# Optimization experiments

Measured on AMD Instinct MI355X. Metric: run time of the kernel, lower is better.

The kernel has to match this reference:

```python
import jax, jax.numpy as jnp
import numpy as np

C, K, D_LLM = 32, 16, 768
B, L, D_MODEL = 8, 512, 256
H, D_KEYS = 8, 32
TEMP = 1.0 / np.sqrt(D_KEYS)


def setup_inputs() -> dict:
    key = jax.random.key(0)
    ks = jax.random.split(key, 8)
    topk = jax.random.normal(ks[0], (C, K, D_LLM), dtype=jnp.float32)
    ts_emb = jax.random.normal(ks[1], (B, L, D_MODEL), dtype=jnp.float32)
    probs = jax.random.uniform(ks[2], (B, L, C), dtype=jnp.float32)
    probs = probs / jnp.sum(probs, axis=-1, keepdims=True)  # soft cluster probabilities
    scale = 0.02  # keep pre-softmax logits in a stable range
    q_proj = jax.random.normal(ks[3], (C, H * D_KEYS, D_MODEL + 1), dtype=jnp.float32) * scale
    k_proj = jax.random.normal(ks[4], (C, H * D_KEYS, D_LLM + 1), dtype=jnp.float32) * scale
    v_proj = jax.random.normal(ks[5], (C, H * D_KEYS, D_LLM + 1), dtype=jnp.float32) * scale
    out_w = jax.random.normal(ks[6], (C, H, D_KEYS, D_LLM), dtype=jnp.float32) * scale
    out_b = jax.random.normal(ks[7], (C, D_LLM), dtype=jnp.float32) * scale
    return {"topk_token_embeddings": topk, "ts_emb": ts_emb, "cluster_probs": probs,
            "q_proj": q_proj, "k_proj": k_proj, "v_proj": v_proj,
            "out_w": out_w, "out_b": out_b}


def reference(topk_token_embeddings, ts_emb, cluster_probs, q_proj, k_proj, v_proj, out_w, out_b):
    b, l, _ = ts_emb.shape
    c, k, d_llm = topk_token_embeddings.shape
    # per-cluster Q/K/V projections (weights have an extra trailing bias column)
    q = jnp.einsum('bld,cgd->blcg', ts_emb, q_proj[..., :-1]) + q_proj[..., -1]
    q = q.reshape(b, l, c, H, D_KEYS)
    kk = jnp.einsum('ckd,cgd->kcg', topk_token_embeddings, k_proj[..., :-1]) + k_proj[..., -1]
    kk = kk.reshape(k, c, H, D_KEYS)
    v = jnp.einsum('ckd,cgd->kcg', topk_token_embeddings, v_proj[..., :-1]) + v_proj[..., -1]
    v = v.reshape(k, c, H, D_KEYS)
    # cross attention over the k retrieved tokens, per cluster and head
    att = jnp.einsum('blchd,kchd->bchlk', q, kk)  # (B,c,H,L,k)
    att = jax.nn.softmax(TEMP * att, axis=-1)  # dropout disabled (eval)
    out_v = jnp.einsum('bchlk,kchd->bclhd', att, v)
    aligned = jnp.einsum('bclhd,chde->blce', out_v, out_w) + out_b  # (B,L,c,d_llm)
    fused = jnp.sum(aligned * cluster_probs[:, :, :, None], axis=-2)  # (B,L,d_llm)
    return fused
```

## Files before the change

kernel.cpp:

```cpp
#include <hip/hip_runtime.h>
#include <hip/hip_bf16.h>

#define C_   32
#define K_   16
#define DLLM 768
#define DM   256
#define H_   8
#define DK   32
#define G_   256
#define BL   4096
#define NN   4096
#define E_   768
#define LDP  4160
#define TEMPF 0.17677669529663687f
#define SCL2  0.2550348647f

typedef __attribute__((ext_vector_type(8))) short bf16x8;
typedef __attribute__((ext_vector_type(4))) float f32x4;
typedef unsigned int u32;

__device__ __forceinline__ unsigned short f2bf(float f) {
    unsigned int u = __float_as_uint(f);
    unsigned int r = (u + 0x7fffu + ((u >> 16) & 1u)) >> 16;
    return (unsigned short)r;
}
__device__ __forceinline__ float bf2f(unsigned int u) {
    return __uint_as_float(u << 16);
}

__device__ __forceinline__ void gl16(const void* g, void* l) {
    __builtin_amdgcn_global_load_lds(
        (const __attribute__((address_space(1))) u32*)g,
        (__attribute__((address_space(3))) u32*)l, 16, 0, 0);
}

__global__ __launch_bounds__(256) void k1_kv(const float* __restrict__ topk,
                                             const float* __restrict__ kp,
                                             const float* __restrict__ vp,
                                             float* __restrict__ kk,
                                             float* __restrict__ vv) {
    const int c  = blockIdx.x;
    const int gq = blockIdx.y;
    const int t = threadIdx.x;
    const int lane = t & 63, w = t >> 6;

    __shared__ float t_l[K_][DLLM];
    {
        const float4* src = reinterpret_cast<const float4*>(topk + (size_t)c * K_ * DLLM);
        float4* dst = reinterpret_cast<float4*>(&t_l[0][0]);
#pragma unroll
        for (int i = 0; i < 12; ++i)
            dst[t + i * 256] = src[t + i * 256];
    }
    __syncthreads();

    const int g0 = gq * 16 + w * 4;
    const int dbase = lane * 4;

    float4 ck[3], cv[3], nk[3], nv[3];
    {
        const float* kpr = kp + (size_t)(c * G_ + g0) * (DLLM + 1);
        const float* vpr = vp + (size_t)(c * G_ + g0) * (DLLM + 1);
#pragma unroll
        for (int r = 0; r < 3; ++r) {
            ck[r] = *reinterpret_cast<const float4*>(kpr + r * 256 + dbase);
            cv[r] = *reinterpret_cast<const float4*>(vpr + r * 256 + dbase);
        }
    }

#pragma unroll
    for (int gi = 0; gi < 4; ++gi) {
        const int g = g0 + gi;
        const float* kpr = kp + (size_t)(c * G_ + g) * (DLLM + 1);
        const float* vpr = vp + (size_t)(c * G_ + g) * (DLLM + 1);
        if (gi < 3) {
            const float* kpn = kpr + (DLLM + 1);
            const float* vpn = vpr + (DLLM + 1);
#pragma unroll
            for (int r = 0; r < 3; ++r) {
                nk[r] = *reinterpret_cast<const float4*>(kpn + r * 256 + dbase);
                nv[r] = *reinterpret_cast<const float4*>(vpn + r * 256 + dbase);
            }
        }
        const float bk = kpr[DLLM], bv = vpr[DLLM];
        float acck[K_] = {}, accv[K_] = {};
#pragma unroll
        for (int r = 0; r < 3; ++r) {
            const int d = r * 256 + dbase;
#pragma unroll
            for (int k = 0; k < K_; ++k) {
                float4 t4 = *reinterpret_cast<const float4*>(&t_l[k][d]);
                acck[k] += ck[r].x * t4.x + ck[r].y * t4.y + ck[r].z * t4.z + ck[r].w * t4.w;
                accv[k] += cv[r].x * t4.x + cv[r].y * t4.y + cv[r].z * t4.z + cv[r].w * t4.w;
            }
        }
#pragma unroll
        for (int s = 32; s >= 1; s >>= 1) {
#pragma unroll
            for (int k = 0; k < K_; ++k) {
                acck[k] += __shfl_xor(acck[k], s);
                accv[k] += __shfl_xor(accv[k], s);
            }
        }
        if (lane == 0) {
#pragma unroll
            for (int k = 0; k < K_; ++k) {
                kk[(size_t)(c * K_ + k) * G_ + g] = acck[k] + bk;
                vv[(size_t)(c * K_ + k) * G_ + g] = accv[k] + bv;
            }
        }
#pragma unroll
        for (int r = 0; r < 3; ++r) { ck[r] = nk[r]; cv[r] = nv[r]; }
    }
}

__global__ __launch_bounds__(256) void k0_cvt(const float* __restrict__ ts,
                                              const float* __restrict__ probs,
                                              const float* __restrict__ outb,
                                              unsigned short* __restrict__ tsb,
                                              unsigned short* __restrict__ P,
                                              unsigned short* __restrict__ VWt) {
    const int bid = blockIdx.x, t = threadIdx.x;
    if (bid < 1024) {
        const int idx = bid * 1024 + t * 4;
        float4 v = *reinterpret_cast<const float4*>(ts + idx);
        uint2 o;
        o.x = f2bf(v.x) | ((unsigned)f2bf(v.y) << 16);
        o.y = f2bf(v.z) | ((unsigned)f2bf(v.w) << 16);
        *reinterpret_cast<uint2*>(tsb + idx) = o;
    } else if (bid < 1056) {
        const int b2 = bid - 1024;
        const int row = b2 * 128 + (t >> 1);
        const int ch = (t & 1) * 16;
        unsigned short o[16];
#pragma unroll
        for (int j = 0; j < 16; ++j) o[j] = f2bf(probs[row * 32 + ch + j]);
        uint4 u0, u1;
        u0.x = o[0] | (o[1] << 16);  u0.y = o[2] | (o[3] << 16);
        u0.z = o[4] | (o[5] << 16);  u0.w = o[6] | (o[7] << 16);
        u1.x = o[8] | (o[9] << 16);  u1.y = o[10] | (o[11] << 16);
        u1.z = o[12] | (o[13] << 16); u1.w = o[14] | (o[15] << 16);
        unsigned short* dst = P + (size_t)row * LDP + 4096 + ch;
        *reinterpret_cast<uint4*>(dst) = u0;
        *reinterpret_cast<uint4*>(dst + 8) = u1;
        uint4 z = {0u, 0u, 0u, 0u};
        unsigned short* pz = P + (size_t)row * LDP + 4128 + ch;
        *reinterpret_cast<uint4*>(pz) = z;
        *reinterpret_cast<uint4*>(pz + 8) = z;
    } else {
        const int idx = (bid - 1056) * 256 + t;
        const int e = idx >> 5, cc = idx & 31;
        VWt[(size_t)e * LDP + 4096 + cc] = f2bf(outb[cc * E_ + e]);
        VWt[(size_t)e * LDP + 4128 + cc] = 0;
    }
}

__global__ __launch_bounds__(768) void k23(const float* __restrict__ qp,
                                           const float* __restrict__ kk,
                                           const float* __restrict__ ow,
                                           const float* __restrict__ vv,
                                           unsigned short* __restrict__ A2t,
                                           float* __restrict__ abias,
                                           unsigned short* __restrict__ VWt) {
    const int c = blockIdx.x, h = blockIdx.y;
    const int t = threadIdx.x;
    __shared__ float kk_l[K_][DK];
    __shared__ float v_l[K_][DK];
    __shared__ float bq_l[DK];
    if (t < 512) {
        int k = t / DK, d = t % DK;
        kk_l[k][d] = kk[(size_t)(c * K_ + k) * G_ + h * DK + d];
        v_l[k][d]  = vv[(size_t)(c * K_ + k) * G_ + h * DK + d];
    }
    if (t < DK)
        bq_l[t] = qp[(size_t)(c * G_ + h * DK + t) * (DM + 1) + DM];
    __syncthreads();
    const int ch = c * H_ + h;
    {
        const int e = t;
        float acc[K_];
#pragma unroll
        for (int k = 0; k < K_; ++k) acc[k] = 0.f;
        for (int d = 0; d < DK; ++d) {
            float w = ow[((size_t)ch * DK + d) * E_ + e];
#pragma unroll
            for (int k = 0; k < K_; ++k) acc[k] += w * v_l[k][d];
        }
#pragma unroll
        for (int k = 0; k < K_; ++k)
            VWt[(size_t)e * LDP + ch * 16 + k] = f2bf(acc[k]);
    }
    if (t < 256) {
        const int m = t;
        float acc[K_];
#pragma unroll
        for (int k = 0; k < K_; ++k) acc[k] = 0.f;
        for (int d = 0; d < DK; ++d) {
            float wq = qp[(size_t)(c * G_ + h * DK + d) * (DM + 1) + m];
#pragma unroll
            for (int k = 0; k < K_; ++k) acc[k] += wq * kk_l[k][d];
        }
#pragma unroll
        for (int k = 0; k < K_; ++k)
            A2t[(size_t)(ch * 16 + k) * DM + m] = f2bf(acc[k] * SCL2);
        if (m < K_) {
            float s = 0.f;
#pragma unroll
            for (int d = 0; d < DK; ++d) s += bq_l[d] * kk_l[m][d];
            abias[ch * 16 + m] = s * SCL2;
        }
    }
}

__global__ __launch_bounds__(256, 2) void k4_att(const unsigned short* __restrict__ A2t,
                                                 const unsigned short* __restrict__ tsb,
                                                 const float* __restrict__ abias,
                                                 const float* __restrict__ probs,
                                                 unsigned short* __restrict__ P) {
    const int n0  = blockIdx.x * 128;
    const int bl0 = blockIdx.y * 256;
    const int t = threadIdx.x;
    const int lane = t & 63, w = t >> 6;
    const int wr = w >> 1, wc = w & 1;
    const int c = lane & 15, g = lane >> 4;
    const int rsl = (c >> 1) & 3;

    __shared__ unsigned short a_l[3][128 * 32];
    __shared__ unsigned short b_l[3][256 * 32];
    __shared__ float ab_l[128];
    __shared__ float pb_l[256];

    if (t < 128) ab_l[t] = abias[n0 + t];
    pb_l[t] = probs[(size_t)(bl0 + t) * C_ + (n0 >> 7)];

    const int srow = t >> 2;
    const int sw = ((t & 3) ^ ((t >> 3) & 3)) * 8;

#define K4_STAGE(buf, kt)                                                         \
    {                                                                             \
        const int col_ = (kt) * 32 + sw;                                          \
        _Pragma("unroll")                                                         \
        for (int j = 0; j < 2; ++j)                                               \
            gl16(A2t + (size_t)(n0 + j * 64 + srow) * DM + col_,                  \
                 &a_l[buf][j * 2048 + t * 8]);                                    \
        _Pragma("unroll")                                                         \
        for (int j = 0; j < 4; ++j)                                               \
            gl16(tsb + (size_t)(bl0 + j * 64 + srow) * DM + col_,                 \
                 &b_l[buf][j * 2048 + t * 8]);                                    \
    }

    K4_STAGE(0, 0)
    K4_STAGE(1, 1)
    asm volatile("s_waitcnt lgkmcnt(0)" ::: "memory");

    f32x4 acc[4][8] = {};

#pragma unroll
    for (int kt = 0; kt < 8; ++kt) {
        const int bcur = kt % 3;
        if (kt < 6) {
            K4_STAGE((kt + 2) % 3, kt + 2)
            asm volatile("s_waitcnt vmcnt(12)" ::: "memory");
        } else if (kt == 6) {
            asm volatile("s_waitcnt vmcnt(6)" ::: "memory");
        } else {
            asm volatile("s_waitcnt vmcnt(0)" ::: "memory");
        }
        asm volatile("s_barrier" ::: "memory");
        bf16x8 af[4], bfr[8];
#pragma unroll
        for (int a = 0; a < 4; ++a)
            af[a] = *reinterpret_cast<const bf16x8*>(
                &a_l[bcur][(wr * 64 + a * 16 + c) * 32 + (g ^ rsl) * 8]);
#pragma unroll
        for (int b = 0; b < 8; ++b)
            bfr[b] = *reinterpret_cast<const bf16x8*>(
                &b_l[bcur][(wc * 128 + b * 16 + c) * 32 + (g ^ rsl) * 8]);
#pragma unroll
        for (int a = 0; a < 4; ++a)
#pragma unroll
            for (int b = 0; b < 8; ++b)
                acc[a][b] = __builtin_amdgcn_mfma_f32_16x16x32_bf16(af[a], bfr[b], acc[a][b], 0, 0, 0);
        if (kt < 7)
            asm volatile("s_barrier" ::: "memory");
    }
#undef K4_STAGE

#pragma unroll
    for (int a = 0; a < 4; ++a) {
        const int nbase = wr * 64 + a * 16 + g * 4;
#pragma unroll
        for (int b = 0; b < 8; ++b) {
            const int bll = wc * 128 + b * 16 + c;
            float e0 = __builtin_amdgcn_exp2f(acc[a][b][0] + ab_l[nbase + 0]);
            float e1 = __builtin_amdgcn_exp2f(acc[a][b][1] + ab_l[nbase + 1]);
            float e2 = __builtin_amdgcn_exp2f(acc[a][b][2] + ab_l[nbase + 2]);
            float e3 = __builtin_amdgcn_exp2f(acc[a][b][3] + ab_l[nbase + 3]);
            float s = (e0 + e1) + (e2 + e3);
            s += __shfl_xor(s, 16);
            s += __shfl_xor(s, 32);
            const float pv = pb_l[bll] * __builtin_amdgcn_rcpf(s);
            unsigned r0, r1;
            float p0 = e0 * pv, p1 = e1 * pv, p2 = e2 * pv, p3 = e3 * pv;
            asm("v_cvt_pk_bf16_f32 %0, %1, %2" : "=v"(r0) : "v"(p0), "v"(p1));
            asm("v_cvt_pk_bf16_f32 %0, %1, %2" : "=v"(r1) : "v"(p2), "v"(p3));
            uint2 o; o.x = r0; o.y = r1;
            *reinterpret_cast<uint2*>(P + (size_t)(bl0 + bll) * LDP + n0 + nbase) = o;
        }
    }
}

__global__ __launch_bounds__(256, 3) void k5_out(const unsigned short* __restrict__ P,
                                                 const unsigned short* __restrict__ VWt,
                                                 unsigned short* __restrict__ part) {
    const int wg = blockIdx.x;
    const int xcd = wg & 7;
    const int local = wg >> 3;
    const int bl0 = (xcd * 4 + (local & 3)) * 128;
    const int e0  = ((local >> 2) & 3) * 192;
    const int ks  = local >> 4;

    const int t = threadIdx.x;
    const int lane = t & 63, w = t >> 6;
    const int wr = w >> 1, wc = w & 1;
    const int c = lane & 15, g = lane >> 4;
    const int rsl = (c >> 1) & 3;

    __shared__ unsigned short a_l[2][128 * 32];
    __shared__ unsigned short b_l[2][192 * 32];

    const int nstart = ks * 704;
    const int nsteps = (ks == 5) ? 20 : 22;

    const int srow = t >> 2;
    const int sw = ((t & 3) ^ ((t >> 3) & 3)) * 8;

#define K5_STAGE(buf, kt)                                                         \
    {                                                                             \
        const int col_ = nstart + (kt) * 32 + sw;                                 \
        _Pragma("unroll")                                                         \
        for (int j = 0; j < 2; ++j)                                               \
            gl16(P + (size_t)(bl0 + j * 64 + srow) * LDP + col_,                  \
                 &a_l[buf][j * 2048 + t * 8]);                                    \
        _Pragma("unroll")                                                         \
        for (int j = 0; j < 3; ++j)                                               \
            gl16(VWt + (size_t)(e0 + j * 64 + srow) * LDP + col_,                 \
                 &b_l[buf][j * 2048 + t * 8]);                                    \
    }

    K5_STAGE(0, 0)

    f32x4 acc[4][6] = {};
    for (int kt = 0; kt < nsteps; ++kt) {
        const int bcur = kt & 1;
        if (kt + 1 < nsteps) {
            K5_STAGE(bcur ^ 1, kt + 1)
            asm volatile("s_waitcnt vmcnt(5)" ::: "memory");
        } else {
            asm volatile("s_waitcnt vmcnt(0)" ::: "memory");
        }
        asm volatile("s_barrier" ::: "memory");
        bf16x8 af[4], bfr[6];
#pragma unroll
        for (int a = 0; a < 4; ++a)
            af[a] = *reinterpret_cast<const bf16x8*>(
                &a_l[bcur][(wr * 64 + a * 16 + c) * 32 + (g ^ rsl) * 8]);
#pragma unroll
        for (int b = 0; b < 6; ++b)
            bfr[b] = *reinterpret_cast<const bf16x8*>(
                &b_l[bcur][(wc * 96 + b * 16 + c) * 32 + (g ^ rsl) * 8]);
#pragma unroll
        for (int a = 0; a < 4; ++a)
#pragma unroll
            for (int b = 0; b < 6; ++b)
                acc[a][b] = __builtin_amdgcn_mfma_f32_16x16x32_bf16(af[a], bfr[b], acc[a][b], 0, 0, 0);
        if (kt + 1 < nsteps)
            asm volatile("s_barrier" ::: "memory");
    }
#undef K5_STAGE

    unsigned short* pp = part + ((size_t)ks * BL + bl0) * E_ + e0;
#pragma unroll
    for (int a = 0; a < 4; ++a)
#pragma unroll
        for (int b = 0; b < 6; ++b)
#pragma unroll
            for (int i = 0; i < 4; ++i)
                pp[(size_t)(wr * 64 + a * 16 + g * 4 + i) * E_ + wc * 96 + b * 16 + c] =
                    f2bf(acc[a][b][i]);
}

__global__ __launch_bounds__(256) void k6_red(const unsigned short* __restrict__ part,
                                              float* __restrict__ out) {
    const size_t base = ((size_t)blockIdx.x * 256 + threadIdx.x) * 8;
    float s[8] = {};
#pragma unroll
    for (int ks = 0; ks < 6; ++ks) {
        uint4 v = *reinterpret_cast<const uint4*>(part + (size_t)ks * (BL * E_) + base);
        const unsigned u[4] = {v.x, v.y, v.z, v.w};
#pragma unroll
        for (int j = 0; j < 4; ++j) {
            s[2 * j]     += bf2f(u[j] & 0xffffu);
            s[2 * j + 1] += bf2f(u[j] >> 16);
        }
    }
    *reinterpret_cast<float4*>(out + base)     = make_float4(s[0], s[1], s[2], s[3]);
    *reinterpret_cast<float4*>(out + base + 4) = make_float4(s[4], s[5], s[6], s[7]);
}

extern "C" void kernel_launch(void* const* d_in, const int* in_sizes, int n_in,
                              void* d_out, int out_size, void* d_ws, size_t ws_size,
                              hipStream_t stream) {
    const float* topk  = (const float*)d_in[0];
    const float* ts    = (const float*)d_in[1];
    const float* probs = (const float*)d_in[2];
    const float* qp    = (const float*)d_in[3];
    const float* kp    = (const float*)d_in[4];
    const float* vp    = (const float*)d_in[5];
    const float* ow    = (const float*)d_in[6];
    const float* ob    = (const float*)d_in[7];
    float* out = (float*)d_out;

    char* wp = (char*)d_ws;
    float* kk            = (float*)wp;           wp += 524288;
    float* vv            = (float*)wp;           wp += 524288;
    float* ab            = (float*)wp;           wp += 16384;
    unsigned short* tsb  = (unsigned short*)wp;  wp += 2097152;
    unsigned short* A2t  = (unsigned short*)wp;  wp += 2097152;
    unsigned short* VWt  = (unsigned short*)wp;  wp += (size_t)E_ * LDP * 2;
    unsigned short* P    = (unsigned short*)wp;  wp += (size_t)BL * LDP * 2;
    unsigned short* part = (unsigned short*)wp;

    k1_kv <<<dim3(32, 16), 256, 0, stream>>>(topk, kp, vp, kk, vv);
    k0_cvt<<<1152,         256, 0, stream>>>(ts, probs, ob, tsb, P, VWt);
    k23   <<<dim3(32, 8),  768, 0, stream>>>(qp, kk, ow, vv, A2t, ab, VWt);
    k4_att<<<dim3(32, 16), 256, 0, stream>>>(A2t, tsb, ab, probs, P);
    k5_out<<<768,          256, 0, stream>>>(P, VWt, part);
    k6_red<<<1536,         256, 0, stream>>>(part, out);
}
```

Before: 113.8 us.

## Use recursive-halving shuffle reduction and prefetch all projection rows in K/V kernel

The K/V projection kernel now replaces its full butterfly reduction, which ran 32 values across 6 shuffle stages and needed 192 shuffles, with a recursive-halving transpose-reduce of 31 shuffles that leaves each lane pair holding one finished output. The outputs are then written by 32 lanes instead of lane 0 alone. All four weight rows and their biases are loaded up front, before the LDS barrier, so global loads overlap the shared-memory fill. A launch-bounds occupancy hint is added, at the cost of more live registers for the prefetched rows.

Result: faster. 109.3 us (-4.0%).

```diff
diff --git a/kernel.cpp b/kernel.cpp
--- a/kernel.cpp
+++ b/kernel.cpp
@@ -34,11 +34,11 @@
         (__attribute__((address_space(3))) u32*)l, 16, 0, 0);
 }
 
-__global__ __launch_bounds__(256) void k1_kv(const float* __restrict__ topk,
-                                             const float* __restrict__ kp,
-                                             const float* __restrict__ vp,
-                                             float* __restrict__ kk,
-                                             float* __restrict__ vv) {
+__global__ __launch_bounds__(256, 2) void k1_kv(const float* __restrict__ topk,
+                                                const float* __restrict__ kp,
+                                                const float* __restrict__ vp,
+                                                float* __restrict__ kk,
+                                                float* __restrict__ vv) {
     const int c  = blockIdx.x;
     const int gq = blockIdx.y;
     const int t = threadIdx.x;
@@ -52,65 +52,80 @@
         for (int i = 0; i < 12; ++i)
             dst[t + i * 256] = src[t + i * 256];
     }
-    __syncthreads();
 
     const int g0 = gq * 16 + w * 4;
     const int dbase = lane * 4;
 
-    float4 ck[3], cv[3], nk[3], nv[3];
-    {
-        const float* kpr = kp + (size_t)(c * G_ + g0) * (DLLM + 1);
-        const float* vpr = vp + (size_t)(c * G_ + g0) * (DLLM + 1);
+    float4 ck[4][3], cv[4][3];
+    float bk[4], bv[4];
+#pragma unroll
+    for (int gi = 0; gi < 4; ++gi) {
+        const float* kpr = kp + (size_t)(c * G_ + g0 + gi) * (DLLM + 1);
+        const float* vpr = vp + (size_t)(c * G_ + g0 + gi) * (DLLM + 1);
 #pragma unroll
         for (int r = 0; r < 3; ++r) {
-            ck[r] = *reinterpret_cast<const float4*>(kpr + r * 256 + dbase);
-            cv[r] = *reinterpret_cast<const float4*>(vpr + r * 256 + dbase);
-        }
-    }
+            ck[gi][r] = *reinterpret_cast<const float4*>(kpr + r * 256 + dbase);
+            cv[gi][r] = *reinterpret_cast<const float4*>(vpr + r * 256 + dbase);
+        }
+        bk[gi] = kpr[DLLM];
+        bv[gi] = vpr[DLLM];
+    }
+    __syncthreads();
 
 #pragma unroll
     for (int gi = 0; gi < 4; ++gi) {
-        const int g = g0 + gi;
-        const float* kpr = kp + (size_t)(c * G_ + g) * (DLLM + 1);
-        const float* vpr = vp + (size_t)(c * G_ + g) * (DLLM + 1);
-        if (gi < 3) {
-            const float* kpn = kpr + (DLLM + 1);
-            const float* vpn = vpr + (DLLM + 1);
-#pragma unroll
-            for (int r = 0; r < 3; ++r) {
-                nk[r] = *reinterpret_cast<const float4*>(kpn + r * 256 + dbase);
-                nv[r] = *reinterpret_cast<const float4*>(vpn + r * 256 + dbase);
-            }
-        }
-        const float bk = kpr[DLLM], bv = vpr[DLLM];
-        float acck[K_] = {}, accv[K_] = {};
+        float acc[32] = {};
 #pragma unroll
         for (int r = 0; r < 3; ++r) {
             const int d = r * 256 + dbase;
 #pragma unroll
             for (int k = 0; k < K_; ++k) {
                 float4 t4 = *reinterpret_cast<const float4*>(&t_l[k][d]);
-                acck[k] += ck[r].x * t4.x + ck[r].y * t4.y + ck[r].z * t4.z + ck[r].w * t4.w;
-                accv[k] += cv[r].x * t4.x + cv[r].y * t4.y + cv[r].z * t4.z + cv[r].w * t4.w;
+                acc[k]      += ck[gi][r].x * t4.x + ck[gi][r].y * t4.y
+                             + ck[gi][r].z * t4.z + ck[gi][r].w * t4.w;
+                acc[k + 16] += cv[gi][r].x * t4.x + cv[gi][r].y * t4.y
+                             + cv[gi][r].z * t4.z + cv[gi][r].w * t4.w;
             }
         }
 #pragma unroll
-        for (int s = 32; s >= 1; s >>= 1) {
-#pragma unroll
-            for (int k = 0; k < K_; ++k) {
-                acck[k] += __shfl_xor(acck[k], s);
-                accv[k] += __shfl_xor(accv[k], s);
-            }
-        }
-        if (lane == 0) {
-#pragma unroll
-            for (int k = 0; k < K_; ++k) {
-                kk[(size_t)(c * K_ + k) * G_ + g] = acck[k] + bk;
-                vv[(size_t)(c * K_ + k) * G_ + g] = accv[k] + bv;
-            }
-        }
-#pragma unroll
-        for (int r = 0; r < 3; ++r) { ck[r] = nk[r]; cv[r] = nv[r]; }
+        for (int j = 0; j < 16; ++j) {
+            float send = (lane & 32) ? acc[j] : acc[j + 16];
+            float r = __shfl_xor(send, 32);
+            acc[j] = ((lane & 32) ? acc[j + 16] : acc[j]) + r;
+        }
+#pragma unroll
+        for (int j = 0; j < 8; ++j) {
+            float send = (lane & 16) ? acc[j] : acc[j + 8];
+            float r = __shfl_xor(send, 16);
+            acc[j] = ((lane & 16) ? acc[j + 8] : acc[j]) + r;
+        }
+#pragma unroll
+        for (int j = 0; j < 4; ++j) {
+            float send = (lane & 8) ? acc[j] : acc[j + 4];
+            float r = __shfl_xor(send, 8);
+            acc[j] = ((lane & 8) ? acc[j + 4] : acc[j]) + r;
+        }
+#pragma unroll
+        for (int j = 0; j < 2; ++j) {
+            float send = (lane & 4) ? acc[j] : acc[j + 2];
+            float r = __shfl_xor(send, 4);
+            acc[j] = ((lane & 4) ? acc[j + 2] : acc[j]) + r;
+        }
+        {
+            float send = (lane & 2) ? acc[0] : acc[1];
+            float r = __shfl_xor(send, 2);
+            acc[0] = ((lane & 2) ? acc[1] : acc[0]) + r;
+        }
+        acc[0] += __shfl_xor(acc[0], 1);
+
+        if ((lane & 1) == 0) {
+            const int mat = lane >> 5;
+            const int k = ((lane >> 4) & 1) * 8 + ((lane >> 3) & 1) * 4
+                        + ((lane >> 2) & 1) * 2 + ((lane >> 1) & 1);
+            float val = acc[0] + (mat ? bv[gi] : bk[gi]);
+            float* dst = mat ? vv : kk;
+            dst[(size_t)(c * K_ + k) * G_ + (g0 + gi)] = val;
+        }
     }
 }
 
```
